# Kernel optimization log

Measured on AMD Instinct MI355X. Metric: run time of the kernel, lower is better.

Reference implementation:

```python
import jax, jax.numpy as jnp
import numpy as np

D_MODEL = 2048
D_STATE = 128
D_CONV = 4
EXPAND = 2
HEADDIM = 64
CHUNK = 64
D_INNER = EXPAND * D_MODEL            # 4096
NHEADS = D_INNER // HEADDIM           # 64
CONV_DIM = D_INNER + 2 * D_STATE      # 4352
D_IN_PROJ = 2 * D_INNER + 2 * D_STATE + NHEADS  # 8512
BATCH, SEQLEN = 2, 2048


def segsum(x):
    """Stable segment sum. x: (..., T) -> (..., T, T)."""
    T = x.shape[-1]
    xx = jnp.broadcast_to(x[..., :, None], x.shape + (T,))  # [.., d, e] = x[.., d]
    mask_lower = jnp.tril(jnp.ones((T, T), dtype=bool), -1)
    s = jnp.cumsum(jnp.where(mask_lower, xx, 0.0), axis=-2)
    mask_diag = jnp.tril(jnp.ones((T, T), dtype=bool), 0)
    return jnp.where(mask_diag, s, -jnp.inf)


def ssd(x, A, Bm, Cm, chunk):
    """x: [b,L,h,p], A: [b,L,h], Bm/Cm: [b,L,n]."""
    b, L, h, p = x.shape
    c = L // chunk
    x = x.reshape(b, c, chunk, h, p)
    A = A.reshape(b, c, chunk, h).transpose(0, 3, 1, 2)     # b h c l
    Bm = Bm.reshape(b, c, chunk, -1)                         # b c l n
    Cm = Cm.reshape(b, c, chunk, -1)
    A_cum = jnp.cumsum(A, axis=-1)                           # b h c l
    Lmat = jnp.exp(segsum(A))                                # b h c l s
    # intra-chunk (diagonal) output
    Y_diag = jnp.einsum('bcln,bcsn,bhcls,bcshp->bclhp', Cm, Bm, Lmat, x)
    # per-chunk states
    decay_states = jnp.exp(A_cum[..., -1:] - A_cum)          # b h c l
    states = jnp.einsum('bcln,bhcl,bclhp->bchpn', Bm, decay_states, x)
    init = jnp.zeros_like(states[:, :1])
    states = jnp.concatenate([init, states], axis=1)         # b (c+1) h p n
    # inter-chunk recurrence via segsum over chunk-level decays
    A_last = jnp.pad(A_cum[..., -1], ((0, 0), (0, 0), (1, 0)))  # b h (c+1)
    decay_chunk = jnp.exp(segsum(A_last))                    # b h (c+1) (c+1)
    new_states = jnp.einsum('bhzc,bchpn->bzhpn', decay_chunk, states)
    states, final_state = new_states[:, :-1], new_states[:, -1]
    # state -> output
    out_decay = jnp.exp(A_cum)                               # b h c l
    Y_off = jnp.einsum('bcln,bchpn,bhcl->bclhp', Cm, states, out_decay)
    return (Y_diag + Y_off).reshape(b, L, h, p), final_state


def setup_inputs() -> dict:
    key = jax.random.key(0)
    ks = jax.random.split(key, 8)
    u = jax.random.normal(ks[0], (BATCH, SEQLEN, D_MODEL), jnp.float32)
    W_in = jax.random.normal(ks[1], (D_MODEL, D_IN_PROJ), jnp.float32) / np.sqrt(D_MODEL).astype(np.float32)
    conv_w = jax.random.normal(ks[2], (CONV_DIM, D_CONV), jnp.float32) * np.sqrt(2.0 / D_CONV).astype(np.float32)
    conv_b = jnp.zeros((CONV_DIM,), jnp.float32)
    dt_bias = jax.random.uniform(ks[3], (NHEADS,), jnp.float32, minval=-2.0, maxval=2.0)
    A_log = jax.random.normal(ks[4], (NHEADS,), jnp.float32) * 0.1
    D_param = jnp.ones((NHEADS,), jnp.float32)
    norm_w = jnp.ones((D_INNER,), jnp.float32)
    W_out = jax.random.normal(ks[5], (D_INNER, D_MODEL), jnp.float32) / np.sqrt(D_INNER).astype(np.float32)
    return {'u': u, 'W_in': W_in, 'conv_w': conv_w, 'conv_b': conv_b,
            'dt_bias': dt_bias, 'A_log': A_log, 'D_param': D_param,
            'norm_w': norm_w, 'W_out': W_out}


def reference(u, W_in, conv_w, conv_b, dt_bias, A_log, D_param, norm_w, W_out):
    b, L, _ = u.shape
    zxbcdt = u @ W_in                                        # [b, L, 2*din + 2*n + h]
    z = zxbcdt[..., :D_INNER]
    xBC = zxbcdt[..., D_INNER:D_INNER + CONV_DIM]
    dt = zxbcdt[..., D_INNER + CONV_DIM:]
    dt = jax.nn.softplus(dt + dt_bias)                       # [b, L, h]
    # causal depthwise conv1d (kernel D_CONV, groups=channels)
    xp = jnp.pad(xBC, ((0, 0), (D_CONV - 1, 0), (0, 0)))
    xBC = sum(xp[:, w:w + L, :] * conv_w[:, w] for w in range(D_CONV)) + conv_b
    xBC = jax.nn.silu(xBC)
    x = xBC[..., :D_INNER]
    Bm = xBC[..., D_INNER:D_INNER + D_STATE]                 # [b, L, n]
    Cm = xBC[..., D_INNER + D_STATE:]                        # [b, L, n]
    x = x.reshape(b, L, NHEADS, HEADDIM)
    A = -jnp.exp(A_log)                                      # [h]
    y, final_state = ssd(x * dt[..., None], A * dt, Bm, Cm, CHUNK)
    y = y + x * D_param[:, None]                             # skip term
    y = y.reshape(b, L, D_INNER)
    # gated RMSNorm (fp32)
    yf = y * jax.nn.silu(z)
    rrms = jax.lax.rsqrt(jnp.mean(yf * yf, axis=-1, keepdims=True) + 1e-5)
    y = yf * rrms * norm_w
    return y @ W_out
```

## Files before the change

kernel.cpp:

```cpp
#include <hip/hip_runtime.h>

typedef unsigned short u16;
typedef __attribute__((ext_vector_type(8))) short bhalf8;
typedef __attribute__((ext_vector_type(4))) float floatx4;

__device__ __forceinline__ u16 f2bf(float f) {
    union { float f; unsigned u; } v; v.f = f;
    unsigned u = v.u;
    unsigned r = u + 0x7fffu + ((u >> 16) & 1u);
    return (u16)(r >> 16);
}
__device__ __forceinline__ float b2f(u16 h) {
    union { unsigned u; float f; } v; v.u = ((unsigned)h) << 16; return v.f;
}
__device__ __forceinline__ void unpack2(unsigned u, float& lo, float& hi) {
    union { unsigned u; float f; } a, b;
    a.u = u << 16; b.u = u & 0xffff0000u;
    lo = a.f; hi = b.f;
}
__device__ __forceinline__ void load_lds16(const void* g, void* l) {
    __builtin_amdgcn_global_load_lds(
        (const __attribute__((address_space(1))) unsigned int*)g,
        (__attribute__((address_space(3))) unsigned int*)l, 16, 0, 0);
}

__global__ void k_f2b4(const float* __restrict__ in, u16* __restrict__ out, int n4) {
    int i = blockIdx.x * 256 + threadIdx.x;
    if (i < n4) {
        float4 v = ((const float4*)in)[i];
        unsigned lo = (unsigned)f2bf(v.x) | ((unsigned)f2bf(v.y) << 16);
        unsigned hi = (unsigned)f2bf(v.z) | ((unsigned)f2bf(v.w) << 16);
        ((uint2*)out)[i] = make_uint2(lo, hi);
    }
}

__global__ void k_transpose_f2b(const float* __restrict__ W, u16* __restrict__ Wt,
                                int K, int N) {
    __shared__ float tile[32][33];
    int nt = blockIdx.x * 32, kt = blockIdx.y * 32;
    int tx = threadIdx.x, ty = threadIdx.y;
    #pragma unroll
    for (int r = 0; r < 32; r += 8) {
        int k = kt + ty + r, n = nt + tx;
        tile[ty + r][tx] = (n < N && k < K) ? W[(size_t)k * N + n] : 0.f;
    }
    __syncthreads();
    #pragma unroll
    for (int r = 0; r < 32; r += 8) {
        int n = nt + ty + r, k = kt + tx;
        Wt[(size_t)n * K + k] = f2bf(tile[tx][ty + r]);
    }
}

template <int EPI>
__global__ __launch_bounds__(256) void gemm_bt(
    const u16* __restrict__ A, const u16* __restrict__ Bt, int M, int N, int K,
    float* __restrict__ outF,
    u16* __restrict__ zb, u16* __restrict__ xbc, float* __restrict__ dtq,
    const float* __restrict__ dt_bias) {
    __shared__ u16 As[2 * 8192];
    __shared__ u16 Bs[2 * 8192];
    int t = threadIdx.x;
    int w = t >> 6, lane = t & 63;
    int m0 = blockIdx.y * 128, n0 = blockIdx.x * 128;
    int wm = (w >> 1) * 64, wn = (w & 1) * 64;
    floatx4 acc[4][4];
    #pragma unroll
    for (int i = 0; i < 4; i++)
        #pragma unroll
        for (int j = 0; j < 4; j++) acc[i][j] = (floatx4){0.f, 0.f, 0.f, 0.f};

    const int nt = K >> 6;
    const int byte0 = (w * 4) * 1024 + lane * 16;

    auto stage = [&](int sel, int k0) {
        #pragma unroll
        for (int i = 0; i < 4; i++) {
            int byte = byte0 + i * 1024;
            int row = byte >> 7;
            int colb = (byte & 127) ^ ((row & 7) << 4);
            load_lds16(A + (size_t)(m0 + row) * K + k0 + (colb >> 1),
                       (char*)As + sel * 16384 + byte);
            load_lds16(Bt + (size_t)(n0 + row) * K + k0 + (colb >> 1),
                       (char*)Bs + sel * 16384 + byte);
        }
    };

    stage(0, 0);
    __syncthreads();
    int cur = 0;
    for (int kt = 0; kt < nt; ++kt) {
        if (kt + 1 < nt) stage(cur ^ 1, (kt + 1) << 6);
        const u16* Ab = As + cur * 8192;
        const u16* Bb = Bs + cur * 8192;
        #pragma unroll
        for (int ks = 0; ks < 2; ks++) {
            int kk = ks * 32 + ((lane >> 4) << 3);
            bhalf8 af[4], bf[4];
            #pragma unroll
            for (int mi = 0; mi < 4; mi++) {
                int row = wm + mi * 16 + (lane & 15);
                int idx = (row * 64 + kk) ^ ((row & 7) << 3);
                af[mi] = *(const bhalf8*)(Ab + idx);
            }
            #pragma unroll
            for (int ni = 0; ni < 4; ni++) {
                int col = wn + ni * 16 + (lane & 15);
                int idx = (col * 64 + kk) ^ ((col & 7) << 3);
                bf[ni] = *(const bhalf8*)(Bb + idx);
            }
            #pragma unroll
            for (int mi = 0; mi < 4; mi++)
                #pragma unroll
                for (int ni = 0; ni < 4; ni++)
                    acc[mi][ni] = __builtin_amdgcn_mfma_f32_16x16x32_bf16(
                        af[mi], bf[ni], acc[mi][ni], 0, 0, 0);
        }
        __syncthreads();
        cur ^= 1;
    }
    #pragma unroll
    for (int mi = 0; mi < 4; mi++) {
        #pragma unroll
        for (int ni = 0; ni < 4; ni++) {
            floatx4 v = acc[mi][ni];
            int col = n0 + wn + ni * 16 + (lane & 15);
            #pragma unroll
            for (int r = 0; r < 4; r++) {
                int row = m0 + wm + mi * 16 + ((lane >> 4) << 2) + r;
                float val = v[r];
                if (EPI == 0) {
                    outF[(size_t)row * N + col] = val;
                } else {
                    if (col < 4096) {
                        zb[(size_t)row * 4096 + col] = f2bf(val);
                    } else if (col < 8448) {
                        xbc[(size_t)row * 4352 + (col - 4096)] = f2bf(val);
                    } else if (col < 8512) {
                        int h = col - 8448;
                        float xv = val + dt_bias[h];
                        float sp = (xv > 20.f) ? xv : log1pf(__expf(xv));
                        dtq[(size_t)row * 64 + h] = sp;
                    }
                }
            }
        }
    }
}

__global__ __launch_bounds__(256) void k_conv(
    const u16* __restrict__ xbc, const float* __restrict__ conv_w,
    const float* __restrict__ conv_b,
    u16* __restrict__ x, u16* __restrict__ Bo, u16* __restrict__ Co) {
    int bid = blockIdx.x;
    int b = bid >> 8, lt = bid & 255;
    int l0 = lt * 8;
    size_t rb = (size_t)(b * 2048) * 4352;
    for (int ch = threadIdx.x; ch < 4352; ch += 256) {
        float w0 = conv_w[ch * 4 + 0], w1 = conv_w[ch * 4 + 1];
        float w2 = conv_w[ch * 4 + 2], w3 = conv_w[ch * 4 + 3];
        float bc = conv_b[ch];
        float h0 = (l0 >= 3) ? b2f(xbc[rb + (size_t)(l0 - 3) * 4352 + ch]) : 0.f;
        float h1 = (l0 >= 2) ? b2f(xbc[rb + (size_t)(l0 - 2) * 4352 + ch]) : 0.f;
        float h2 = (l0 >= 1) ? b2f(xbc[rb + (size_t)(l0 - 1) * 4352 + ch]) : 0.f;
        #pragma unroll
        for (int i = 0; i < 8; i++) {
            int l = l0 + i;
            float xc = b2f(xbc[rb + (size_t)l * 4352 + ch]);
            float acc = bc + w0 * h0 + w1 * h1 + w2 * h2 + w3 * xc;
            float v = acc / (1.f + __expf(-acc));
            int row = b * 2048 + l;
            if (ch < 4096) {
                x[(size_t)row * 4096 + ch] = f2bf(v);
            } else if (ch < 4224) {
                Bo[(size_t)row * 128 + (ch - 4096)] = f2bf(v);
            } else {
                Co[(size_t)row * 128 + (ch - 4224)] = f2bf(v);
            }
            h0 = h1; h1 = h2; h2 = xc;
        }
    }
}

__global__ void k_dtprep(const float* __restrict__ dtq, const float* __restrict__ A_log,
                         float* __restrict__ acum, float* __restrict__ Tc) {
    int bc = blockIdx.x;
    int h = threadIdx.x;
    float A = -__expf(A_log[h]);
    float s = 0.f;
    #pragma unroll
    for (int l = 0; l < 64; l++) {
        int row = bc * 64 + l;
        s += A * dtq[row * 64 + h];
        acum[(size_t)row * 64 + h] = s;
    }
    int b = bc >> 5, c = bc & 31;
    Tc[(b * 64 + h) * 32 + c] = s;
}

__global__ __launch_bounds__(256) void k_G(const u16* __restrict__ Bo, const u16* __restrict__ Co,
                                           float* __restrict__ G) {
    int bc = blockIdx.x;
    int lq = blockIdx.y;
    __shared__ float BsT[128][68];
    __shared__ float Cs[16][132];
    int t = threadIdx.x;
    for (int idx = t; idx < 64 * 128; idx += 256) {
        int r = idx >> 7, n = idx & 127;
        BsT[n][r] = b2f(Bo[(size_t)(bc * 64 + r) * 128 + n]);
    }
    for (int idx = t; idx < 16 * 128; idx += 256) {
        int r = idx >> 7, n = idx & 127;
        Cs[r][n] = b2f(Co[(size_t)(bc * 64 + lq * 16 + r) * 128 + n]);
    }
    __syncthreads();
    int lr = t >> 4, sq = t & 15;
    int l = lq * 16 + lr;
    float a[4] = {0.f, 0.f, 0.f, 0.f};
    for (int n = 0; n < 128; n++) {
        float cv = Cs[lr][n];
        const float4* bp = (const float4*)&BsT[n][sq * 4];
        float4 b0 = bp[0];
        a[0] += cv * b0.x; a[1] += cv * b0.y; a[2] += cv * b0.z; a[3] += cv * b0.w;
    }
    size_t gb = ((size_t)bc * 64 + l) * 64 + sq * 4;
    #pragma unroll
    for (int i = 0; i < 4; i++) G[gb + i] = a[i];
}

__global__ __launch_bounds__(256) void k_diag(
    const u16* __restrict__ xb, const u16* __restrict__ Bo,
    const float* __restrict__ G, const float* __restrict__ acum,
    const float* __restrict__ dtq,
    u16* __restrict__ y, u16* __restrict__ cs) {
    int bc = blockIdx.x, h = blockIdx.y;
    __shared__ u16 XT[4096];
    __shared__ u16 Pl[4096];
    __shared__ u16 BTd[8192];
    __shared__ float ac[64], dec[64], dts[64];
    int t = threadIdx.x, w = t >> 6, lane = t & 63;
    if (t < 64) {
        ac[t] = acum[(size_t)(bc * 64 + t) * 64 + h];
        dts[t] = dtq[(size_t)(bc * 64 + t) * 64 + h];
    }
    __syncthreads();
    if (t < 64) dec[t] = __expf(ac[63] - ac[t]);
    for (int idx = t; idx < 4096; idx += 256) {
        int s = idx >> 6, p = idx & 63;
        float v = b2f(xb[(size_t)(bc * 64 + s) * 4096 + h * 64 + p]) * dts[s];
        XT[(p << 6) + (s ^ ((p & 7) << 3))] = f2bf(v);
    }
    for (int idx = t; idx < 4096; idx += 256) {
        int l = idx >> 6, s = idx & 63;
        float v = (s <= l) ? __expf(ac[l] - ac[s]) * G[((size_t)bc * 64 + l) * 64 + s] : 0.f;
        Pl[(l << 6) + (s ^ ((l & 7) << 3))] = f2bf(v);
    }
    __syncthreads();
    for (int idx = t; idx < 8192; idx += 256) {
        int l = idx >> 7, n = idx & 127;
        float v = b2f(Bo[(size_t)(bc * 64 + l) * 128 + n]) * dec[l];
        BTd[(n << 6) + (l ^ ((n & 7) << 3))] = f2bf(v);
    }
    __syncthreads();
    {
        floatx4 accY[4];
        #pragma unroll
        for (int ni = 0; ni < 4; ni++) accY[ni] = (floatx4){0.f, 0.f, 0.f, 0.f};
        int row = (w << 4) + (lane & 15);
        #pragma unroll
        for (int ks = 0; ks < 2; ks++) {
            int k = (ks << 5) + ((lane >> 4) << 3);
            int kx = k ^ ((row & 7) << 3);
            bhalf8 af = *(const bhalf8*)(Pl + (row << 6) + kx);
            #pragma unroll
            for (int ni = 0; ni < 4; ni++) {
                int pr = (ni << 4) + (lane & 15);
                bhalf8 bf = *(const bhalf8*)(XT + (pr << 6) + kx);
                accY[ni] = __builtin_amdgcn_mfma_f32_16x16x32_bf16(af, bf, accY[ni], 0, 0, 0);
            }
        }
        #pragma unroll
        for (int ni = 0; ni < 4; ni++) {
            int col = (ni << 4) + (lane & 15);
            #pragma unroll
            for (int r = 0; r < 4; r++) {
                int l = (w << 4) + ((lane >> 4) << 2) + r;
                y[(size_t)(bc * 64 + l) * 4096 + h * 64 + col] = f2bf(accY[ni][r]);
            }
        }
    }
    {
        floatx4 accS[8];
        #pragma unroll
        for (int ni = 0; ni < 8; ni++) accS[ni] = (floatx4){0.f, 0.f, 0.f, 0.f};
        int prow = (w << 4) + (lane & 15);
        #pragma unroll
        for (int ks = 0; ks < 2; ks++) {
            int k = (ks << 5) + ((lane >> 4) << 3);
            int kx = k ^ ((prow & 7) << 3);
            bhalf8 af = *(const bhalf8*)(XT + (prow << 6) + kx);
            #pragma unroll
            for (int ni = 0; ni < 8; ni++) {
                int nr = (ni << 4) + (lane & 15);
                bhalf8 bf = *(const bhalf8*)(BTd + (nr << 6) + kx);
                accS[ni] = __builtin_amdgcn_mfma_f32_16x16x32_bf16(af, bf, accS[ni], 0, 0, 0);
            }
        }
        #pragma unroll
        for (int ni = 0; ni < 8; ni++) {
            int n = (ni << 4) + (lane & 15);
            #pragma unroll
            for (int r = 0; r < 4; r++) {
                int p = (w << 4) + ((lane >> 4) << 2) + r;
                cs[((size_t)(bc * 64 + h) * 64 + p) * 128 + n] = f2bf(accS[ni][r]);
            }
        }
    }
}

__global__ __launch_bounds__(256) void k_scan(u16* __restrict__ cs, const float* __restrict__ Tc) {
    int bid = blockIdx.x;
    int bh = bid >> 5, pb = bid & 31;
    int b = bh >> 6, h = bh & 63;
    int pn = pb * 256 + threadIdx.x;
    const float* Tp = Tc + bh * 32;
    size_t stride = (size_t)64 * 8192;
    size_t base = (((size_t)(b * 32) * 64) + h) * 8192 + pn;
    float v[32];
    #pragma unroll
    for (int c = 0; c < 32; c++) v[c] = b2f(cs[base + (size_t)c * stride]);
    float P = 0.f;
    #pragma unroll
    for (int c = 0; c < 32; c++) {
        float tmp = v[c];
        cs[base + (size_t)c * stride] = f2bf(P);
        P = __expf(Tp[c]) * P + tmp;
    }
}

__global__ __launch_bounds__(256) void k_yoff(
    const u16* __restrict__ Co, const u16* __restrict__ cs,
    const float* __restrict__ acum, u16* __restrict__ y) {
    int bc = blockIdx.x, h = blockIdx.y;
    __shared__ u16 Cl[8192];
    __shared__ u16 Sl[8192];
    __shared__ float od[64];
    int t = threadIdx.x, w = t >> 6, lane = t & 63;
    for (int idx = t; idx < 8192; idx += 256) {
        int l = idx >> 7, n = idx & 127;
        Cl[(l << 7) + (n ^ ((l & 15) << 3))] = Co[(size_t)(bc * 64 + l) * 128 + n];
    }
    size_t pbase = ((size_t)bc * 64 + h) * 8192;
    for (int idx = t; idx < 8192; idx += 256) {
        int p = idx >> 7, n = idx & 127;
        Sl[(p << 7) + (n ^ ((p & 15) << 3))] = cs[pbase + idx];
    }
    if (t < 64) od[t] = __expf(acum[(size_t)(bc * 64 + t) * 64 + h]);
    __syncthreads();
    floatx4 acc[4];
    #pragma unroll
    for (int ni = 0; ni < 4; ni++) acc[ni] = (floatx4){0.f, 0.f, 0.f, 0.f};
    int lrow = (w << 4) + (lane & 15);
    #pragma unroll
    for (int ks = 0; ks < 4; ks++) {
        int k = (ks << 5) + ((lane >> 4) << 3);
        int kx = k ^ ((lrow & 15) << 3);
        bhalf8 af = *(const bhalf8*)(Cl + (lrow << 7) + kx);
        #pragma unroll
        for (int ni = 0; ni < 4; ni++) {
            int pr = (ni << 4) + (lane & 15);
            bhalf8 bf = *(const bhalf8*)(Sl + (pr << 7) + kx);
            acc[ni] = __builtin_amdgcn_mfma_f32_16x16x32_bf16(af, bf, acc[ni], 0, 0, 0);
        }
    }
    #pragma unroll
    for (int ni = 0; ni < 4; ni++) {
        int col = (ni << 4) + (lane & 15);
        #pragma unroll
        for (int r = 0; r < 4; r++) {
            int l = (w << 4) + ((lane >> 4) << 2) + r;
            size_t yi = (size_t)(bc * 64 + l) * 4096 + h * 64 + col;
            y[yi] = f2bf(b2f(y[yi]) + od[l] * acc[ni][r]);
        }
    }
}

__global__ __launch_bounds__(256) void k_norm(
    const u16* __restrict__ y, const u16* __restrict__ x, const u16* __restrict__ z,
    const float* __restrict__ D_param, const float* __restrict__ norm_w,
    u16* __restrict__ ynorm) {
    int row = blockIdx.x;
    int t = threadIdx.x;
    size_t base = (size_t)row * 4096 + (size_t)t * 16;
    float yv[16], xf[16], zf[16];
    {
        uint4 a = ((const uint4*)(y + base))[0];
        uint4 b = ((const uint4*)(y + base))[1];
        unpack2(a.x, yv[0], yv[1]); unpack2(a.y, yv[2], yv[3]);
        unpack2(a.z, yv[4], yv[5]); unpack2(a.w, yv[6], yv[7]);
        unpack2(b.x, yv[8], yv[9]); unpack2(b.y, yv[10], yv[11]);
        unpack2(b.z, yv[12], yv[13]); unpack2(b.w, yv[14], yv[15]);
    }
    {
        uint4 a = ((const uint4*)(x + base))[0];
        uint4 b = ((const uint4*)(x + base))[1];
        unpack2(a.x, xf[0], xf[1]); unpack2(a.y, xf[2], xf[3]);
        unpack2(a.z, xf[4], xf[5]); unpack2(a.w, xf[6], xf[7]);
        unpack2(b.x, xf[8], xf[9]); unpack2(b.y, xf[10], xf[11]);
        unpack2(b.z, xf[12], xf[13]); unpack2(b.w, xf[14], xf[15]);
    }
    {
        uint4 a = ((const uint4*)(z + base))[0];
        uint4 b = ((const uint4*)(z + base))[1];
        unpack2(a.x, zf[0], zf[1]); unpack2(a.y, zf[2], zf[3]);
        unpack2(a.z, zf[4], zf[5]); unpack2(a.w, zf[6], zf[7]);
        unpack2(b.x, zf[8], zf[9]); unpack2(b.y, zf[10], zf[11]);
        unpack2(b.z, zf[12], zf[13]); unpack2(b.w, zf[14], zf[15]);
    }
    float D = D_param[t >> 2];
    float vals[16], ss = 0.f;
    #pragma unroll
    for (int j = 0; j < 16; j++) {
        float v = yv[j] + xf[j] * D;
        float zz = zf[j];
        float yf = v * (zz / (1.f + __expf(-zz)));
        vals[j] = yf;
        ss += yf * yf;
    }
    #pragma unroll
    for (int o = 32; o > 0; o >>= 1) ss += __shfl_down(ss, o, 64);
    __shared__ float red[4];
    if ((t & 63) == 0) red[t >> 6] = ss;
    __syncthreads();
    float tot = red[0] + red[1] + red[2] + red[3];
    float rr = rsqrtf(tot * (1.f / 4096.f) + 1e-5f);
    unsigned o32[8];
    #pragma unroll
    for (int j = 0; j < 8; j++) {
        float lo = vals[2 * j] * rr * norm_w[t * 16 + 2 * j];
        float hi = vals[2 * j + 1] * rr * norm_w[t * 16 + 2 * j + 1];
        o32[j] = (unsigned)f2bf(lo) | ((unsigned)f2bf(hi) << 16);
    }
    uint4 w0, w1;
    w0.x = o32[0]; w0.y = o32[1]; w0.z = o32[2]; w0.w = o32[3];
    w1.x = o32[4]; w1.y = o32[5]; w1.z = o32[6]; w1.w = o32[7];
    ((uint4*)(ynorm + base))[0] = w0;
    ((uint4*)(ynorm + base))[1] = w1;
}

extern "C" void kernel_launch(void* const* d_in, const int* in_sizes, int n_in,
                              void* d_out, int out_size, void* d_ws, size_t ws_size,
                              hipStream_t stream) {
    const float* u       = (const float*)d_in[0];
    const float* W_in    = (const float*)d_in[1];
    const float* conv_w  = (const float*)d_in[2];
    const float* conv_b  = (const float*)d_in[3];
    const float* dt_bias = (const float*)d_in[4];
    const float* A_log   = (const float*)d_in[5];
    const float* D_param = (const float*)d_in[6];
    const float* norm_w  = (const float*)d_in[7];
    const float* W_out   = (const float*)d_in[8];
    float* out = (float*)d_out;

    const size_t REGION = (size_t)134217728;
    size_t need = REGION
                + (size_t)33554432
                + (size_t)33554432
                + (size_t)1048576
                + (size_t)1048576
                + (size_t)1048576
                + (size_t)16384
                + (size_t)1048576
                + (size_t)1048576
                + (size_t)33554432;
    if (ws_size < need) return;

    char* ws = (char*)d_ws;
    u16*   ubf   = (u16*)(ws);
    u16*   WinT  = (u16*)(ws + 16777216);
    u16*   xbc   = (u16*)(ws + 16777216 + 35651584);
    u16*   cs    = (u16*)(ws);
    u16*   WoutT = (u16*)(ws);
    u16*   ynorm = (u16*)(ws + 16777216);
    char* p = ws + REGION;
    u16*   zb    = (u16*)p;            p += 33554432;
    u16*   xb    = (u16*)p;            p += 33554432;
    u16*   Bo    = (u16*)p;            p += 1048576;
    u16*   Co    = (u16*)p;            p += 1048576;
    float* acum  = (float*)p;          p += 1048576;
    float* Tc    = (float*)p;          p += 16384;
    float* G     = (float*)p;          p += 1048576;
    float* dtq   = (float*)p;          p += 1048576;
    u16*   yb    = (u16*)p;            p += 33554432;

    k_f2b4<<<8192, 256, 0, stream>>>(u, ubf, 4096 * 2048 / 4);
    k_transpose_f2b<<<dim3(268, 64), dim3(32, 8), 0, stream>>>(W_in, WinT, 2048, 8512);
    gemm_bt<1><<<dim3(67, 32), 256, 0, stream>>>(ubf, WinT, 4096, 8576, 2048,
                                                 nullptr, zb, xbc, dtq, dt_bias);
    k_conv<<<512, 256, 0, stream>>>(xbc, conv_w, conv_b, xb, Bo, Co);
    k_dtprep<<<64, 64, 0, stream>>>(dtq, A_log, acum, Tc);
    k_G<<<dim3(64, 4), 256, 0, stream>>>(Bo, Co, G);
    k_diag<<<dim3(64, 64), 256, 0, stream>>>(xb, Bo, G, acum, dtq, yb, cs);
    k_scan<<<4096, 256, 0, stream>>>(cs, Tc);
    k_yoff<<<dim3(64, 64), 256, 0, stream>>>(Co, cs, acum, yb);
    k_transpose_f2b<<<dim3(64, 128), dim3(32, 8), 0, stream>>>(W_out, WoutT, 4096, 2048);
    k_norm<<<4096, 256, 0, stream>>>(yb, xb, zb, D_param, norm_w, ynorm);
    gemm_bt<0><<<dim3(16, 32), 256, 0, stream>>>(ynorm, WoutT, 4096, 2048, 4096,
                                                 out, nullptr, nullptr, nullptr, nullptr);
    (void)in_sizes; (void)n_in; (void)out_size;
}
```

Measured before the change: 607.0 us.

## Vectorize conv loads/stores, batch two heads per yoff block, raise MFMA priority

The depthwise conv kernel now processes channel pairs, using 32-bit loads and packed bf16 stores and float4 weight loads, which halves memory instructions. k_yoff now handles two heads per block, reusing the C tile staged in shared memory and halving the grid. The GEMM raises wave priority around its MFMA cluster with s_setprio. These are three unrelated tweaks. The larger shared-memory footprint in yoff could lower occupancy.

```diff
diff --git a/kernel.cpp b/kernel.cpp
--- a/kernel.cpp
+++ b/kernel.cpp
@@ -109,12 +109,14 @@
                 int idx = (col * 64 + kk) ^ ((col & 7) << 3);
                 bf[ni] = *(const bhalf8*)(Bb + idx);
             }
+            __builtin_amdgcn_s_setprio(1);
             #pragma unroll
             for (int mi = 0; mi < 4; mi++)
                 #pragma unroll
                 for (int ni = 0; ni < 4; ni++)
                     acc[mi][ni] = __builtin_amdgcn_mfma_f32_16x16x32_bf16(
                         af[mi], bf[ni], acc[mi][ni], 0, 0, 0);
+            __builtin_amdgcn_s_setprio(0);
         }
         __syncthreads();
         cur ^= 1;
@@ -155,29 +157,37 @@
     int bid = blockIdx.x;
     int b = bid >> 8, lt = bid & 255;
     int l0 = lt * 8;
-    size_t rb = (size_t)(b * 2048) * 4352;
-    for (int ch = threadIdx.x; ch < 4352; ch += 256) {
-        float w0 = conv_w[ch * 4 + 0], w1 = conv_w[ch * 4 + 1];
-        float w2 = conv_w[ch * 4 + 2], w3 = conv_w[ch * 4 + 3];
-        float bc = conv_b[ch];
-        float h0 = (l0 >= 3) ? b2f(xbc[rb + (size_t)(l0 - 3) * 4352 + ch]) : 0.f;
-        float h1 = (l0 >= 2) ? b2f(xbc[rb + (size_t)(l0 - 2) * 4352 + ch]) : 0.f;
-        float h2 = (l0 >= 1) ? b2f(xbc[rb + (size_t)(l0 - 1) * 4352 + ch]) : 0.f;
+    const unsigned* xb32 = (const unsigned*)xbc;
+    size_t rb = (size_t)(b * 2048) * 2176;
+    for (int cp = threadIdx.x; cp < 2176; cp += 256) {
+        int ch = cp << 1;
+        const float4* wp = (const float4*)(conv_w + ch * 4);
+        float4 wA = wp[0], wB = wp[1];
+        float bcA = conv_b[ch], bcB = conv_b[ch + 1];
+        float h0A = 0.f, h1A = 0.f, h2A = 0.f, h0B = 0.f, h1B = 0.f, h2B = 0.f;
+        if (l0 >= 3) unpack2(xb32[rb + (size_t)(l0 - 3) * 2176 + cp], h0A, h0B);
+        if (l0 >= 2) unpack2(xb32[rb + (size_t)(l0 - 2) * 2176 + cp], h1A, h1B);
+        if (l0 >= 1) unpack2(xb32[rb + (size_t)(l0 - 1) * 2176 + cp], h2A, h2B);
         #pragma unroll
         for (int i = 0; i < 8; i++) {
             int l = l0 + i;
-            float xc = b2f(xbc[rb + (size_t)l * 4352 + ch]);
-            float acc = bc + w0 * h0 + w1 * h1 + w2 * h2 + w3 * xc;
-            float v = acc / (1.f + __expf(-acc));
+            float xcA, xcB;
+            unpack2(xb32[rb + (size_t)l * 2176 + cp], xcA, xcB);
+            float aA = bcA + wA.x * h0A + wA.y * h1A + wA.z * h2A + wA.w * xcA;
+            float aB = bcB + wB.x * h0B + wB.y * h1B + wB.z * h2B + wB.w * xcB;
+            float vA = aA / (1.f + __expf(-aA));
+            float vB = aB / (1.f + __expf(-aB));
             int row = b * 2048 + l;
+            unsigned pk = (unsigned)f2bf(vA) | ((unsigned)f2bf(vB) << 16);
             if (ch < 4096) {
-                x[(size_t)row * 4096 + ch] = f2bf(v);
+                ((unsigned*)x)[(size_t)row * 2048 + cp] = pk;
             } else if (ch < 4224) {
-                Bo[(size_t)row * 128 + (ch - 4096)] = f2bf(v);
+                ((unsigned*)Bo)[(size_t)row * 64 + (cp - 2048)] = pk;
             } else {
-                Co[(size_t)row * 128 + (ch - 4224)] = f2bf(v);
-            }
-            h0 = h1; h1 = h2; h2 = xc;
+                ((unsigned*)Co)[(size_t)row * 64 + (cp - 2112)] = pk;
+            }
+            h0A = h1A; h1A = h2A; h2A = xcA;
+            h0B = h1B; h1B = h2B; h2B = xcB;
         }
     }
 }
@@ -341,46 +351,56 @@
 __global__ __launch_bounds__(256) void k_yoff(
     const u16* __restrict__ Co, const u16* __restrict__ cs,
     const float* __restrict__ acum, u16* __restrict__ y) {
-    int bc = blockIdx.x, h = blockIdx.y;
+    int bc = blockIdx.x;
+    int h0 = blockIdx.y << 1;
     __shared__ u16 Cl[8192];
-    __shared__ u16 Sl[8192];
-    __shared__ float od[64];
+    __shared__ u16 Sl[2][8192];
+    __shared__ float od[2][64];
     int t = threadIdx.x, w = t >> 6, lane = t & 63;
     for (int idx = t; idx < 8192; idx += 256) {
         int l = idx >> 7, n = idx & 127;
         Cl[(l << 7) + (n ^ ((l & 15) << 3))] = Co[(size_t)(bc * 64 + l) * 128 + n];
     }
-    size_t pbase = ((size_t)bc * 64 + h) * 8192;
-    for (int idx = t; idx < 8192; idx += 256) {
-        int p = idx >> 7, n = idx & 127;
-        Sl[(p << 7) + (n ^ ((p & 15) << 3))] = cs[pbase + idx];
-    }
-    if (t < 64) od[t] = __expf(acum[(size_t)(bc * 64 + t) * 64 + h]);
-    __syncthreads();
-    floatx4 acc[4];
-    #pragma unroll
-    for (int ni = 0; ni < 4; ni++) acc[ni] = (floatx4){0.f, 0.f, 0.f, 0.f};
+    #pragma unroll
+    for (int j = 0; j < 2; j++) {
+        size_t pbase = ((size_t)bc * 64 + (h0 + j)) * 8192;
+        for (int idx = t; idx < 8192; idx += 256) {
+            int p = idx >> 7, n = idx & 127;
+            Sl[j][(p << 7) + (n ^ ((p & 15) << 3))] = cs[pbase + idx];
+        }
+    }
+    if (t < 128) {
+        int j = t >> 6, l = t & 63;
+        od[j][l] = __expf(acum[(size_t)(bc * 64 + l) * 64 + h0 + j]);
+    }
+    __syncthreads();
     int lrow = (w << 4) + (lane & 15);
     #pragma unroll
-    for (int ks = 0; ks < 4; ks++) {
-        int k = (ks << 5) + ((lane >> 4) << 3);
-        int kx = k ^ ((lrow & 15) << 3);
-        bhalf8 af = *(const bhalf8*)(Cl + (lrow << 7) + kx);
+    for (int j = 0; j < 2; j++) {
+        floatx4 acc[4];
+        #pragma unroll
+        for (int ni = 0; ni < 4; ni++) acc[ni] = (floatx4){0.f, 0.f, 0.f, 0.f};
+        #pragma unroll
+        for (int ks = 0; ks < 4; ks++) {
+            int k = (ks << 5) + ((lane >> 4) << 3);
+            int kx = k ^ ((lrow & 15) << 3);
+            bhalf8 af = *(const bhalf8*)(Cl + (lrow << 7) + kx);
+            #pragma unroll
+            for (int ni = 0; ni < 4; ni++) {
+                int pr = (ni << 4) + (lane & 15);
+                bhalf8 bf = *(const bhalf8*)(Sl[j] + (pr << 7) + kx);
+                acc[ni] = __builtin_amdgcn_mfma_f32_16x16x32_bf16(af, bf, acc[ni], 0, 0, 0);
+            }
+        }
         #pragma unroll
         for (int ni = 0; ni < 4; ni++) {
-            int pr = (ni << 4) + (lane & 15);
-            bhalf8 bf = *(const bhalf8*)(Sl + (pr << 7) + kx);
-            acc[ni] = __builtin_amdgcn_mfma_f32_16x16x32_bf16(af, bf, acc[ni], 0, 0, 0);
-        }
-    }
-    #pragma unroll
-    for (int ni = 0; ni < 4; ni++) {
-        int col = (ni << 4) + (lane & 15);
-        #pragma unroll
-        for (int r = 0; r < 4; r++) {
-            int l = (w << 4) + ((lane >> 4) << 2) + r;
-            size_t yi = (size_t)(bc * 64 + l) * 4096 + h * 64 + col;
-            y[yi] = f2bf(b2f(y[yi]) + od[l] * acc[ni][r]);
+            int col = (ni << 4) + (lane & 15);
+            #pragma unroll
+            for (int r = 0; r < 4; r++) {
+                int l = (w << 4) + ((lane >> 4) << 2) + r;
+                size_t yi = (size_t)(bc * 64 + l) * 4096 + (h0 + j) * 64 + col;
+                y[yi] = f2bf(b2f(y[yi]) + od[j][l] * acc[ni][r]);
+            }
         }
     }
 }
@@ -502,7 +522,7 @@
     k_G<<<dim3(64, 4), 256, 0, stream>>>(Bo, Co, G);
     k_diag<<<dim3(64, 64), 256, 0, stream>>>(xb, Bo, G, acum, dtq, yb, cs);
     k_scan<<<4096, 256, 0, stream>>>(cs, Tc);
-    k_yoff<<<dim3(64, 64), 256, 0, stream>>>(Co, cs, acum, yb);
+    k_yoff<<<dim3(64, 32), 256, 0, stream>>>(Co, cs, acum, yb);
     k_transpose_f2b<<<dim3(64, 128), dim3(32, 8), 0, stream>>>(W_out, WoutT, 4096, 2048);
     k_norm<<<4096, 256, 0, stream>>>(yb, xb, zb, D_param, norm_w, ynorm);
     gemm_bt<0><<<dim3(16, 32), 256, 0, stream>>>(ynorm, WoutT, 4096, 2048, 4096,
```

Result: faster. 590.2 us (-2.8%).
